# Kernel optimization log

Hardware: AMD Instinct MI355X
Metric: run time of the kernel (lower is better)

## Reference

```python
import jax, jax.numpy as jnp
import numpy as np

B, S, D, H = 2, 4096, 1024, 16
HD = D // H  # 64


def setup_inputs() -> dict:
    key = jax.random.key(0)
    ks = jax.random.split(key, 6)
    return {
        "x": jax.random.normal(ks[0], (B, S, D), dtype=jnp.float32),
        "mask": jax.random.normal(ks[1], (B, S, S), dtype=jnp.float32),
        "Wqkv": jax.random.normal(ks[2], (D, 3 * D), dtype=jnp.float32) * 0.02,
        "bqkv": jax.random.normal(ks[3], (3 * D,), dtype=jnp.float32) * 0.02,
        "Wo": jax.random.normal(ks[4], (D, D), dtype=jnp.float32) * 0.02,
        "bo": jax.random.normal(ks[5], (D,), dtype=jnp.float32) * 0.02,
    }


def reference(x, mask, Wqkv, bqkv, Wo, bo):
    b, s, d = x.shape
    # fused QKV projection: [B,S,3D]
    qkv = jnp.einsum('bsd,de->bse', x, Wqkv) + bqkv
    # [B,S,H,3*HD] -> [B,H,S,3*HD]
    qkv = qkv.reshape(b, s, H, 3 * HD).transpose(0, 2, 1, 3)
    q, k, v = jnp.split(qkv, 3, axis=-1)  # each [B,H,S,HD]
    scale = 1.0 / jnp.sqrt(jnp.asarray(HD, dtype=x.dtype))
    scores = jnp.einsum('bhqe,bhke->bhqk', q, k) * scale  # [B,H,S,S]
    scores = scores + mask[:, None, :, :]  # additive mask broadcast over heads
    attn = jax.nn.softmax(scores, axis=-1)
    values = jnp.einsum('bhqk,bhke->bhqe', attn, v)  # [B,H,S,HD]
    # NOTE: faithful to original TF code: reshape WITHOUT transposing heads back
    values = values.reshape(b, s, d)
    out = jnp.einsum('bsd,de->bse', values, Wo) + bo
    return out
```

## Files before the change

### kernel.cpp

```cpp
#include <hip/hip_runtime.h>
#include <hip/hip_bf16.h>

#define DEV __device__ __forceinline__

typedef unsigned short u16;
typedef __attribute__((ext_vector_type(4))) float f32x4;
typedef __attribute__((ext_vector_type(8))) short s16x8;

static constexpr int Bc = 2, Hc = 16, Sc = 4096, Dc = 1024, HDc = 64;

DEV u16 f2bf(float f) {
  unsigned x = __float_as_uint(f);
  x += 0x7FFFu + ((x >> 16) & 1u);
  return (u16)(x >> 16);
}
DEV float bf2f(u16 u) { return __uint_as_float(((unsigned)u) << 16); }

DEV unsigned cvtpk_bf16(float lo, float hi) {
  unsigned r;
  asm("v_cvt_pk_bf16_f32 %0, %1, %2" : "=v"(r) : "v"(lo), "v"(hi));
  return r;
}

DEV void gload_lds16(const void* g, void* l) {
  __builtin_amdgcn_global_load_lds((const __attribute__((address_space(1))) void*)g,
                                   (__attribute__((address_space(3))) void*)l, 16, 0, 0);
}

DEV f32x4 mfma16(s16x8 a, s16x8 b, f32x4 c) {
  return __builtin_amdgcn_mfma_f32_16x16x32_bf16(a, b, c, 0, 0, 0);
}

DEV f32x4 fzero4() { f32x4 v; v[0] = v[1] = v[2] = v[3] = 0.f; return v; }

__global__ void cvt_f32_bf16(const float* __restrict__ in, u16* __restrict__ out, size_t n) {
  size_t i = ((size_t)blockIdx.x * blockDim.x + threadIdx.x) * 4;
  size_t stride = (size_t)gridDim.x * blockDim.x * 4;
  for (; i < n; i += stride) {
    float4 v = *(const float4*)(in + i);
    u16 a = f2bf(v.x), b = f2bf(v.y), c = f2bf(v.z), d = f2bf(v.w);
    *(ushort4*)(out + i) = make_ushort4(a, b, c, d);
  }
}

__global__ void transpose_cvt(const float* __restrict__ in, u16* __restrict__ out, int R, int C) {
  __shared__ u16 t[64][72];
  int nct = C >> 6;
  int tr = blockIdx.x / nct, tc = blockIdx.x % nct;
  int r0 = tr << 6, c0 = tc << 6;
  int lr = threadIdx.x >> 2;
  int lc0 = (threadIdx.x & 3) << 4;
  const float* src = in + (size_t)(r0 + lr) * C + c0 + lc0;
#pragma unroll
  for (int j = 0; j < 16; j += 4) {
    float4 v = *(const float4*)(src + j);
    t[lr][lc0 + j + 0] = f2bf(v.x);
    t[lr][lc0 + j + 1] = f2bf(v.y);
    t[lr][lc0 + j + 2] = f2bf(v.z);
    t[lr][lc0 + j + 3] = f2bf(v.w);
  }
  __syncthreads();
  u16* dst = out + (size_t)(c0 + lr) * R + r0 + lc0;
#pragma unroll
  for (int j = 0; j < 16; j += 4) {
    u16 a = t[lc0 + j + 0][lr], b = t[lc0 + j + 1][lr], c = t[lc0 + j + 2][lr], d = t[lc0 + j + 3][lr];
    *(ushort4*)(dst + j) = make_ushort4(a, b, c, d);
  }
}

template <int MODE>
__global__ __launch_bounds__(256, 2) void gemm128(
    const u16* __restrict__ A, const u16* __restrict__ BT, const float* __restrict__ bias,
    void* __restrict__ out0, u16* __restrict__ out1, u16* __restrict__ out2,
    int N, int K, int grid_n) {
  __shared__ u16 Al[128 * 64];
  __shared__ u16 Bl[128 * 64];
  int bid = blockIdx.x;
  int bn = bid % grid_n, bm = bid / grid_n;
  int m0 = bm * 128, n0 = bn * 128;
  int tid = threadIdx.x, lane = tid & 63, wid = tid >> 6;
  int wm = wid >> 1, wn = wid & 1;
  int fr = lane & 15, fg = lane >> 4;

  f32x4 acc[4][4];
#pragma unroll
  for (int mi = 0; mi < 4; ++mi)
#pragma unroll
    for (int ni = 0; ni < 4; ++ni) acc[mi][ni] = fzero4();

  for (int kt = 0; kt < K; kt += 64) {
    const u16* Ag = A + (size_t)m0 * K + kt;
    const u16* Bg = BT + (size_t)n0 * K + kt;
#pragma unroll
    for (int it = 0; it < 4; ++it) {
      int L = it * 4096 + wid * 1024 + lane * 16;
      int row = L >> 7;
      int sch = ((L >> 4) & 7) ^ (row & 7);
      gload_lds16(Ag + (size_t)row * K + sch * 8, (char*)Al + it * 4096 + wid * 1024);
      gload_lds16(Bg + (size_t)row * K + sch * 8, (char*)Bl + it * 4096 + wid * 1024);
    }
    __syncthreads();
#pragma unroll
    for (int c = 0; c < 2; ++c) {
      s16x8 af[4], bfr[4];
#pragma unroll
      for (int mi = 0; mi < 4; ++mi) {
        int row = wm * 64 + mi * 16 + fr;
        int ch = (c * 4 + fg) ^ (row & 7);
        af[mi] = *(const s16x8*)((const char*)Al + row * 128 + ch * 16);
      }
#pragma unroll
      for (int ni = 0; ni < 4; ++ni) {
        int row = wn * 64 + ni * 16 + fr;
        int ch = (c * 4 + fg) ^ (row & 7);
        bfr[ni] = *(const s16x8*)((const char*)Bl + row * 128 + ch * 16);
      }
#pragma unroll
      for (int mi = 0; mi < 4; ++mi)
#pragma unroll
        for (int ni = 0; ni < 4; ++ni) acc[mi][ni] = mfma16(af[mi], bfr[ni], acc[mi][ni]);
    }
    __syncthreads();
  }

  if constexpr (MODE == 0) {
    u16* qb = (u16*)out0;
    u16* kb = out1;
    u16* vT = out2;
#pragma unroll
    for (int ni = 0; ni < 4; ++ni) {
      int n = n0 + wn * 64 + ni * 16 + fr;
      float bv = bias[n];
      int h = n / 192;
      int c = n % 192;
      int part = c >> 6;
      int e = c & 63;
#pragma unroll
      for (int mi = 0; mi < 4; ++mi) {
        int m = m0 + wm * 64 + mi * 16 + fg * 4;
        int b = m >> 12;
        int s = m & 4095;
        size_t bh = (size_t)b * Hc + h;
        if (part == 2) {
          u16 a0 = f2bf(acc[mi][ni][0] + bv), a1 = f2bf(acc[mi][ni][1] + bv);
          u16 a2 = f2bf(acc[mi][ni][2] + bv), a3 = f2bf(acc[mi][ni][3] + bv);
          *(ushort4*)(vT + ((bh * HDc + e) * (size_t)Sc + s)) = make_ushort4(a0, a1, a2, a3);
        } else {
          u16* dst = (part == 0 ? qb : kb) + ((bh * Sc + s) * (size_t)HDc + e);
#pragma unroll
          for (int r = 0; r < 4; ++r) dst[(size_t)r * HDc] = f2bf(acc[mi][ni][r] + bv);
        }
      }
    }
  } else {
    float* O = (float*)out0;
#pragma unroll
    for (int ni = 0; ni < 4; ++ni) {
      int n = n0 + wn * 64 + ni * 16 + fr;
      float bv = bias[n];
#pragma unroll
      for (int mi = 0; mi < 4; ++mi) {
        int m = m0 + wm * 64 + mi * 16 + fg * 4;
#pragma unroll
        for (int r = 0; r < 4; ++r) O[(size_t)(m + r) * N + n] = acc[mi][ni][r] + bv;
      }
    }
  }
}

__global__ __launch_bounds__(256, 2) void attn_kernel(
    const u16* __restrict__ qb, const u16* __restrict__ kb, const u16* __restrict__ vT,
    const float* __restrict__ maskp, u16* __restrict__ vals) {
  __shared__ u16 Kl[2][64 * 64];
  __shared__ u16 Vl[2][64 * 64];
  __shared__ char Pl[4 * 16 * 144];

  int bid = ((blockIdx.x & 7) << 8) | (blockIdx.x >> 3);
  int h = bid & 15, b = (bid >> 4) & 1, qt = bid >> 5;
  int lane = threadIdx.x & 63, wid = threadIdx.x >> 6;
  int fr = lane & 15, fg = lane >> 4;
  size_t bh = (size_t)b * Hc + h;
  int q0 = qt * 64;
  int q = q0 + wid * 16 + fr;

  const u16* Qrow = qb + ((bh * Sc) + q) * (size_t)HDc;
  s16x8 qa0 = *(const s16x8*)(Qrow + fg * 8);
  s16x8 qa1 = *(const s16x8*)(Qrow + 32 + fg * 8);

  f32x4 o[4];
#pragma unroll
  for (int ef = 0; ef < 4; ++ef) o[ef] = fzero4();
  float mrun = -1e30f, lrun = 0.f;

  const u16* Kg = kb + bh * (size_t)Sc * HDc;
  const u16* Vg = vT + bh * (size_t)HDc * Sc;
  char* pw = (char*)Pl + wid * 2304 + fr * 144;
  const float SCALE = 0.125f;
  const float LOG2E = 1.44269504088896340736f;

  int L0 = wid * 1024 + lane * 16;
  int L1 = 4096 + wid * 1024 + lane * 16;
  int row0 = L0 >> 7, row1 = L1 >> 7;
  int sch0s = ((L0 >> 4) & 7) ^ (row0 & 7);
  int sch1s = ((L1 >> 4) & 7) ^ (row1 & 7);
  const u16* KgS0 = Kg + (size_t)row0 * HDc + sch0s * 8;
  const u16* KgS1 = Kg + (size_t)row1 * HDc + sch1s * 8;
  const u16* VgS0 = Vg + (size_t)row0 * Sc + sch0s * 8;
  const u16* VgS1 = Vg + (size_t)row1 * Sc + sch1s * 8;
  int ldsA = wid * 1024;
  int ldsB = 4096 + wid * 1024;

  int ch0 = fg ^ (fr & 7);
  int ch1 = (4 + fg) ^ (fr & 7);
  int kroff0 = fr * 128 + ch0 * 16;
  int kroff1 = fr * 128 + ch1 * 16;

  const float* mk = maskp + ((size_t)b * Sc + q) * Sc;

  gload_lds16(KgS0, (char*)Kl[0] + ldsA);
  gload_lds16(KgS1, (char*)Kl[0] + ldsB);
  gload_lds16(VgS0, (char*)Vl[0] + ldsA);
  gload_lds16(VgS1, (char*)Vl[0] + ldsB);
  __syncthreads();

  for (int kt = 0; kt < Sc / 64; ++kt) {
    int cur = kt & 1;
    if (kt < Sc / 64 - 1) {
      int nxt = cur ^ 1;
      size_t ko = (size_t)(kt + 1) * 64 * HDc;
      size_t vo = (size_t)(kt + 1) * 64;
      gload_lds16(KgS0 + ko, (char*)Kl[nxt] + ldsA);
      gload_lds16(KgS1 + ko, (char*)Kl[nxt] + ldsB);
      gload_lds16(VgS0 + vo, (char*)Vl[nxt] + ldsA);
      gload_lds16(VgS1 + vo, (char*)Vl[nxt] + ldsB);
    }

    const float* mrow = mk + kt * 64 + fg * 4;
    float4 mf0 = *(const float4*)(mrow);
    float4 mf1 = *(const float4*)(mrow + 16);
    float4 mf2 = *(const float4*)(mrow + 32);
    float4 mf3 = *(const float4*)(mrow + 48);

    const char* Kc = (const char*)Kl[cur];
    f32x4 sa[4];
#pragma unroll
    for (int f = 0; f < 4; ++f) sa[f] = fzero4();
    __builtin_amdgcn_s_setprio(1);
#pragma unroll
    for (int f = 0; f < 4; ++f) {
      s16x8 kf = *(const s16x8*)(Kc + f * 2048 + kroff0);
      sa[f] = mfma16(kf, qa0, sa[f]);
    }
#pragma unroll
    for (int f = 0; f < 4; ++f) {
      s16x8 kf = *(const s16x8*)(Kc + f * 2048 + kroff1);
      sa[f] = mfma16(kf, qa1, sa[f]);
    }
    __builtin_amdgcn_s_setprio(0);

    float t[4][4];
#pragma unroll
    for (int r = 0; r < 4; ++r) {
      t[0][r] = fmaf(sa[0][r], SCALE, (&mf0.x)[r]);
      t[1][r] = fmaf(sa[1][r], SCALE, (&mf1.x)[r]);
      t[2][r] = fmaf(sa[2][r], SCALE, (&mf2.x)[r]);
      t[3][r] = fmaf(sa[3][r], SCALE, (&mf3.x)[r]);
    }

    float x0 = fmaxf(fmaxf(t[0][0], t[0][1]), t[0][2]);
    float x1 = fmaxf(fmaxf(t[0][3], t[1][0]), t[1][1]);
    float x2 = fmaxf(fmaxf(t[1][2], t[1][3]), t[2][0]);
    float x3 = fmaxf(fmaxf(t[2][1], t[2][2]), t[2][3]);
    float x4 = fmaxf(fmaxf(t[3][0], t[3][1]), t[3][2]);
    float mt = fmaxf(fmaxf(fmaxf(x0, x1), x2), fmaxf(fmaxf(x3, x4), t[3][3]));
    mt = fmaxf(mt, __shfl_xor(mt, 16, 64));
    mt = fmaxf(mt, __shfl_xor(mt, 32, 64));

    if (!__all(mt <= mrun + 8.0f)) {
      float mnew = fmaxf(mrun, mt);
      float al = __builtin_amdgcn_exp2f((mrun - mnew) * LOG2E);
      mrun = mnew;
      lrun *= al;
#pragma unroll
      for (int ef = 0; ef < 4; ++ef) o[ef] *= al;
    }

    float nm = -mrun * LOG2E;
    float p[4][4];
    float ss0 = 0.f, ss1 = 0.f;
#pragma unroll
    for (int f = 0; f < 4; ++f) {
      float p0 = __builtin_amdgcn_exp2f(fmaf(t[f][0], LOG2E, nm));
      float p1 = __builtin_amdgcn_exp2f(fmaf(t[f][1], LOG2E, nm));
      float p2 = __builtin_amdgcn_exp2f(fmaf(t[f][2], LOG2E, nm));
      float p3 = __builtin_amdgcn_exp2f(fmaf(t[f][3], LOG2E, nm));
      p[f][0] = p0; p[f][1] = p1; p[f][2] = p2; p[f][3] = p3;
      ss0 += (p0 + p1);
      ss1 += (p2 + p3);
    }
    float ssum = ss0 + ss1;
    ssum += __shfl_xor(ssum, 16, 64);
    ssum += __shfl_xor(ssum, 32, 64);
    lrun += ssum;

#pragma unroll
    for (int f = 0; f < 4; ++f) {
      uint2 pk;
      pk.x = cvtpk_bf16(p[f][0], p[f][1]);
      pk.y = cvtpk_bf16(p[f][2], p[f][3]);
      *(uint2*)(pw + f * 32 + fg * 8) = pk;
    }

    const char* Vc = (const char*)Vl[cur];
    s16x8 pa0 = *(const s16x8*)(pw + fg * 16);
    s16x8 pa1 = *(const s16x8*)(pw + 64 + fg * 16);
    __builtin_amdgcn_s_setprio(1);
#pragma unroll
    for (int ef = 0; ef < 4; ++ef) {
      s16x8 vf = *(const s16x8*)(Vc + ef * 2048 + kroff0);
      o[ef] = mfma16(vf, pa0, o[ef]);
    }
#pragma unroll
    for (int ef = 0; ef < 4; ++ef) {
      s16x8 vf = *(const s16x8*)(Vc + ef * 2048 + kroff1);
      o[ef] = mfma16(vf, pa1, o[ef]);
    }
    __builtin_amdgcn_s_setprio(0);

    __syncthreads();
  }

  float inv = 1.f / lrun;
  u16* vbase = vals + (size_t)b * Sc * Dc + (size_t)h * Sc * HDc + (size_t)q * HDc;
#pragma unroll
  for (int ef = 0; ef < 4; ++ef) {
    ushort4 ov = make_ushort4(f2bf(o[ef][0] * inv), f2bf(o[ef][1] * inv),
                              f2bf(o[ef][2] * inv), f2bf(o[ef][3] * inv));
    *(ushort4*)(vbase + ef * 16 + fg * 4) = ov;
  }
}

extern "C" void kernel_launch(void* const* d_in, const int* in_sizes, int n_in,
                              void* d_out, int out_size, void* d_ws, size_t ws_size,
                              hipStream_t stream) {
  (void)in_sizes; (void)n_in; (void)out_size; (void)ws_size;
  const float* x    = (const float*)d_in[0];
  const float* mask = (const float*)d_in[1];
  const float* Wqkv = (const float*)d_in[2];
  const float* bqkv = (const float*)d_in[3];
  const float* Wo   = (const float*)d_in[4];
  const float* bo   = (const float*)d_in[5];
  float* out = (float*)d_out;
  char* ws = (char*)d_ws;

  u16* xb    = (u16*)(ws + 0);
  u16* wqkvT = (u16*)(ws + 16777216);
  u16* woT   = (u16*)(ws + 23068672);
  u16* qb    = (u16*)(ws + 25165824);
  u16* kb    = (u16*)(ws + 41943040);
  u16* vT    = (u16*)(ws + 58720256);
  u16* vals  = (u16*)(ws + 75497472);

  cvt_f32_bf16<<<dim3(2048), dim3(256), 0, stream>>>(x, xb, (size_t)8388608);
  transpose_cvt<<<dim3(768), dim3(256), 0, stream>>>(Wqkv, wqkvT, 1024, 3072);
  transpose_cvt<<<dim3(256), dim3(256), 0, stream>>>(Wo, woT, 1024, 1024);

  gemm128<0><<<dim3(1536), dim3(256), 0, stream>>>(xb, wqkvT, bqkv, (void*)qb, kb, vT,
                                                   3072, 1024, 24);
  attn_kernel<<<dim3(2048), dim3(256), 0, stream>>>(qb, kb, vT, mask, vals);
  gemm128<1><<<dim3(512), dim3(256), 0, stream>>>(vals, woT, bo, (void*)out, nullptr, nullptr,
                                                  1024, 1024, 8);
}
```

Measured before the change: 451.7 us.

## Replace double-buffered direct-to-LDS loads with register-staged single buffer, raise occupancy

Switches K/V tile staging from double-buffered global-to-LDS async loads to a single LDS buffer filled from registers that are prefetched one tile ahead, with an extra barrier before each store. Halving LDS use lets launch bounds request 6 blocks per CU instead of 2, so more waves can hide latency. The cost is more registers per thread, an added __syncthreads per iteration, and explicit register-to-LDS writes in place of the direct global-to-LDS path.

Result: slower. 489.2 us (+8.3%).

```diff
diff --git a/kernel.cpp b/kernel.cpp
--- a/kernel.cpp
+++ b/kernel.cpp
@@ -168,16 +168,17 @@
   }
 }
 
-__global__ __launch_bounds__(256, 2) void attn_kernel(
+__global__ __launch_bounds__(256, 6) void attn_kernel(
     const u16* __restrict__ qb, const u16* __restrict__ kb, const u16* __restrict__ vT,
     const float* __restrict__ maskp, u16* __restrict__ vals) {
-  __shared__ u16 Kl[2][64 * 64];
-  __shared__ u16 Vl[2][64 * 64];
+  __shared__ u16 Kl[64 * 64];
+  __shared__ u16 Vl[64 * 64];
   __shared__ char Pl[4 * 16 * 144];
 
   int bid = ((blockIdx.x & 7) << 8) | (blockIdx.x >> 3);
   int h = bid & 15, b = (bid >> 4) & 1, qt = bid >> 5;
-  int lane = threadIdx.x & 63, wid = threadIdx.x >> 6;
+  int tid = threadIdx.x;
+  int lane = tid & 63, wid = tid >> 6;
   int fr = lane & 15, fg = lane >> 4;
   size_t bh = (size_t)b * Hc + h;
   int q0 = qt * 64;
@@ -198,42 +199,40 @@
   const float SCALE = 0.125f;
   const float LOG2E = 1.44269504088896340736f;
 
-  int L0 = wid * 1024 + lane * 16;
-  int L1 = 4096 + wid * 1024 + lane * 16;
-  int row0 = L0 >> 7, row1 = L1 >> 7;
-  int sch0s = ((L0 >> 4) & 7) ^ (row0 & 7);
-  int sch1s = ((L1 >> 4) & 7) ^ (row1 & 7);
-  const u16* KgS0 = Kg + (size_t)row0 * HDc + sch0s * 8;
-  const u16* KgS1 = Kg + (size_t)row1 * HDc + sch1s * 8;
-  const u16* VgS0 = Vg + (size_t)row0 * Sc + sch0s * 8;
-  const u16* VgS1 = Vg + (size_t)row1 * Sc + sch1s * 8;
-  int ldsA = wid * 1024;
-  int ldsB = 4096 + wid * 1024;
-
-  int ch0 = fg ^ (fr & 7);
-  int ch1 = (4 + fg) ^ (fr & 7);
-  int kroff0 = fr * 128 + ch0 * 16;
-  int kroff1 = fr * 128 + ch1 * 16;
+  int e8 = tid & 7;
+  int r5 = tid >> 3;
+  int rr = r5 & 7;
+  int swc = (e8 ^ rr) << 4;
+  int ldsw0 = (0 * 32 + r5) * 128 + swc;
+  int ldsw1 = (1 * 32 + r5) * 128 + swc;
+  const u16* KgL0 = Kg + (size_t)(0 * 32 + r5) * HDc + e8 * 8;
+  const u16* KgL1 = Kg + (size_t)(1 * 32 + r5) * HDc + e8 * 8;
+  const u16* VgL0 = Vg + (size_t)(0 * 32 + r5) * Sc + e8 * 8;
+  const u16* VgL1 = Vg + (size_t)(1 * 32 + r5) * Sc + e8 * 8;
+
+  int kroff0 = fr * 128 + ((fg ^ (fr & 7)) << 4);
+  int kroff1 = fr * 128 + (((4 + fg) ^ (fr & 7)) << 4);
 
   const float* mk = maskp + ((size_t)b * Sc + q) * Sc;
 
-  gload_lds16(KgS0, (char*)Kl[0] + ldsA);
-  gload_lds16(KgS1, (char*)Kl[0] + ldsB);
-  gload_lds16(VgS0, (char*)Vl[0] + ldsA);
-  gload_lds16(VgS1, (char*)Vl[0] + ldsB);
+  {
+    uint4 k0 = *(const uint4*)(KgL0);
+    uint4 k1 = *(const uint4*)(KgL1);
+    uint4 v0 = *(const uint4*)(VgL0);
+    uint4 v1 = *(const uint4*)(VgL1);
+    *(uint4*)((char*)Kl + ldsw0) = k0;
+    *(uint4*)((char*)Kl + ldsw1) = k1;
+    *(uint4*)((char*)Vl + ldsw0) = v0;
+    *(uint4*)((char*)Vl + ldsw1) = v1;
+  }
   __syncthreads();
 
   for (int kt = 0; kt < Sc / 64; ++kt) {
-    int cur = kt & 1;
-    if (kt < Sc / 64 - 1) {
-      int nxt = cur ^ 1;
-      size_t ko = (size_t)(kt + 1) * 64 * HDc;
-      size_t vo = (size_t)(kt + 1) * 64;
-      gload_lds16(KgS0 + ko, (char*)Kl[nxt] + ldsA);
-      gload_lds16(KgS1 + ko, (char*)Kl[nxt] + ldsB);
-      gload_lds16(VgS0 + vo, (char*)Vl[nxt] + ldsA);
-      gload_lds16(VgS1 + vo, (char*)Vl[nxt] + ldsB);
-    }
+    int ktn = (kt < Sc / 64 - 1) ? kt + 1 : kt;
+    uint4 kn0 = *(const uint4*)(KgL0 + (size_t)ktn * 4096);
+    uint4 kn1 = *(const uint4*)(KgL1 + (size_t)ktn * 4096);
+    uint4 vn0 = *(const uint4*)(VgL0 + (size_t)ktn * 64);
+    uint4 vn1 = *(const uint4*)(VgL1 + (size_t)ktn * 64);
 
     const float* mrow = mk + kt * 64 + fg * 4;
     float4 mf0 = *(const float4*)(mrow);
@@ -241,19 +240,18 @@
     float4 mf2 = *(const float4*)(mrow + 32);
     float4 mf3 = *(const float4*)(mrow + 48);
 
-    const char* Kc = (const char*)Kl[cur];
     f32x4 sa[4];
 #pragma unroll
     for (int f = 0; f < 4; ++f) sa[f] = fzero4();
     __builtin_amdgcn_s_setprio(1);
 #pragma unroll
     for (int f = 0; f < 4; ++f) {
-      s16x8 kf = *(const s16x8*)(Kc + f * 2048 + kroff0);
+      s16x8 kf = *(const s16x8*)((const char*)Kl + f * 2048 + kroff0);
       sa[f] = mfma16(kf, qa0, sa[f]);
     }
 #pragma unroll
     for (int f = 0; f < 4; ++f) {
-      s16x8 kf = *(const s16x8*)(Kc + f * 2048 + kroff1);
+      s16x8 kf = *(const s16x8*)((const char*)Kl + f * 2048 + kroff1);
       sa[f] = mfma16(kf, qa1, sa[f]);
     }
     __builtin_amdgcn_s_setprio(0);
@@ -311,22 +309,26 @@
       *(uint2*)(pw + f * 32 + fg * 8) = pk;
     }
 
-    const char* Vc = (const char*)Vl[cur];
     s16x8 pa0 = *(const s16x8*)(pw + fg * 16);
     s16x8 pa1 = *(const s16x8*)(pw + 64 + fg * 16);
     __builtin_amdgcn_s_setprio(1);
 #pragma unroll
     for (int ef = 0; ef < 4; ++ef) {
-      s16x8 vf = *(const s16x8*)(Vc + ef * 2048 + kroff0);
+      s16x8 vf = *(const s16x8*)((const char*)Vl + ef * 2048 + kroff0);
       o[ef] = mfma16(vf, pa0, o[ef]);
     }
 #pragma unroll
     for (int ef = 0; ef < 4; ++ef) {
-      s16x8 vf = *(const s16x8*)(Vc + ef * 2048 + kroff1);
+      s16x8 vf = *(const s16x8*)((const char*)Vl + ef * 2048 + kroff1);
       o[ef] = mfma16(vf, pa1, o[ef]);
     }
     __builtin_amdgcn_s_setprio(0);
 
+    __syncthreads();
+    *(uint4*)((char*)Kl + ldsw0) = kn0;
+    *(uint4*)((char*)Kl + ldsw1) = kn1;
+    *(uint4*)((char*)Vl + ldsw0) = vn0;
+    *(uint4*)((char*)Vl + ldsw1) = vn1;
     __syncthreads();
   }
 
```
